# Kernel optimization log

Measured on AMD Instinct MI355X. Metric: run time of the kernel, lower is better.

Reference implementation:

```python
import jax, jax.numpy as jnp
import numpy as np

B, C, F_IN, F_OUT = 4096, 63, 250, 250
NEG_SLOPE = 0.2  # GATConv default negative_slope


def setup_inputs() -> dict:
    key = jax.random.key(0)
    ks = jax.random.split(key, 5)
    return {
        "x": jax.random.normal(ks[0], (B, 1, C, F_IN), dtype=jnp.float32),
        "W": jax.random.normal(ks[1], (F_IN, F_OUT), dtype=jnp.float32) / np.sqrt(F_IN),
        "att_src": jax.random.normal(ks[2], (F_OUT,), dtype=jnp.float32) / np.sqrt(F_OUT),
        "att_dst": jax.random.normal(ks[3], (F_OUT,), dtype=jnp.float32) / np.sqrt(F_OUT),
        "bias": jax.random.normal(ks[4], (F_OUT,), dtype=jnp.float32) * 0.01,
    }


def reference(x, W, att_src, att_dst, bias):
    # x: [B, 1, C, F_in] -> per-batch graph of C=63 nodes, fully connected
    # (all i!=j edges plus GATConv's default self-loops => dense C x C attention).
    h = jnp.einsum("bcf,fo->bco", x[:, 0], W)          # [B, C, F_out] node embeddings
    a_s = jnp.einsum("bco,o->bc", h, att_src)           # per-source score
    a_d = jnp.einsum("bco,o->bc", h, att_dst)           # per-destination score
    # e[b, dst, src] = leakyrelu(a_s[src] + a_d[dst]); softmax over sources per dst
    e = jax.nn.leaky_relu(a_s[:, None, :] + a_d[:, :, None], NEG_SLOPE)  # [B, C, C]
    alpha = jax.nn.softmax(e, axis=-1)
    out = jnp.einsum("bds,bso->bdo", alpha, h) + bias   # [B, C, F_out]
    return out[:, None]                                  # [B, 1, C, F_out]
```

## Files before the change

### kernel.cpp

```cpp
#include <hip/hip_runtime.h>
#include <hip/hip_bf16.h>

typedef __bf16 bf16;
typedef __attribute__((ext_vector_type(8))) __bf16 bf16x8;
typedef __attribute__((ext_vector_type(2))) __bf16 bf16x2;
typedef __attribute__((ext_vector_type(4))) float f32x4;
typedef __attribute__((ext_vector_type(4))) unsigned int uint4v;

#define C_NODES 63
#define F_DIM   250
#define NEG_SLOPE 0.2f
#define BS 8

#define ROWB      1040
#define SLAB      0
#define OFF_AS    65536
#define OFF_AD    65792
#define ALPHA_B   66048
#define LDS_BYTES 74240

__device__ __forceinline__ int swz(int a) { return a ^ ((a >> 3) & 0x70); }

typedef const __attribute__((address_space(1))) void* gas_t;
typedef __attribute__((address_space(3))) void* las_t;
__device__ __forceinline__ void dma16(const void* g, void* l) {
    __builtin_amdgcn_global_load_lds((gas_t)g, (las_t)l, 16, 0, 0);
}

__device__ __forceinline__ void bar_lgkm() {
    asm volatile("s_waitcnt lgkmcnt(0)" ::: "memory");
    __builtin_amdgcn_s_barrier();
    __builtin_amdgcn_sched_barrier(0);
}

extern "C" __global__ __launch_bounds__(256)
void gat_prep(const float* __restrict__ W, const float* __restrict__ att_src,
              const float* __restrict__ att_dst, bf16* __restrict__ Wp) {
    int i = blockIdx.x * 256 + threadIdx.x;
    int tile = i >> 9;
    int ln   = (i >> 3) & 63;
    int j    = i & 7;
    int kt = tile >> 4, nt = tile & 15;
    int k = kt * 32 + (ln >> 4) * 8 + j;
    int n = nt * 16 + (ln & 15);
    float v = 0.f;
    if (k < F_DIM) {
        if (n < F_DIM) {
            v = W[k * F_DIM + n];
        } else if (n == F_DIM || n == F_DIM + 1) {
            const float* att = (n == F_DIM) ? att_src : att_dst;
            float s = 0.f;
            for (int o = 0; o < F_DIM; ++o) s = fmaf(W[k * F_DIM + o], att[o], s);
            v = s;
        }
    }
    Wp[i] = (bf16)v;
}

extern "C" __global__ __launch_bounds__(512, 4)
void gat_main(const float* __restrict__ x, const bf16* __restrict__ Wp,
              const float* __restrict__ bias, float* __restrict__ out)
{
    __shared__ __align__(16) unsigned char smem[LDS_BYTES];
    const int tid  = threadIdx.x;
    const int lane = tid & 63;
    const int w    = tid >> 6;
    const int fl   = lane & 15;
    const int fh   = lane >> 4;
    const int b0   = blockIdx.x * BS;

    const bf16x8* wpv = (const bf16x8*)Wp;

    float bv0, bv1;
    { int f = w * 32 + fl;      bv0 = (f < F_DIM) ? bias[f] : 0.f;
      f += 16;                  bv1 = (f < F_DIM) ? bias[f] : 0.f; }

    if (tid < 63) {
        *(unsigned long long*)(smem + SLAB + tid * ROWB + 1000) = 0ull;
        *(f32x4*)(smem + SLAB + tid * ROWB + 1008) = (f32x4){0.f, 0.f, 0.f, 0.f};
    }

    {
        const float* xb = x + (size_t)b0 * (C_NODES * F_DIM);
        float2 tl = {0.f, 0.f};
        if (tid < 63) tl = *(const float2*)(xb + tid * F_DIM + 248);
#pragma unroll
        for (int rr = 0; rr < 8; ++rr) {
            int r = w * 8 + rr;
            if (r < 63 && lane < 62)
                dma16(xb + r * F_DIM + lane * 4, smem + SLAB + r * ROWB);
        }
        if (tid < 63) *(float2*)(smem + SLAB + tid * ROWB + 992) = tl;
    }
    asm volatile("s_waitcnt vmcnt(0)" ::: "memory");
    bar_lgkm();

#pragma unroll 1
    for (int i = 0; i < BS; ++i) {
        const int b = b0 + i;
        const float* xnext = x + (size_t)(b + 1) * (C_NODES * F_DIM);

        float2 tl = {0.f, 0.f};
        if (i + 1 < BS && tid < 63) tl = *(const float2*)(xnext + tid * F_DIM + 248);

        f32x4 acc[4][2];
#pragma unroll
        for (int mt = 0; mt < 4; ++mt) {
            acc[mt][0] = (f32x4){0.f, 0.f, 0.f, 0.f};
            acc[mt][1] = (f32x4){0.f, 0.f, 0.f, 0.f};
        }
#pragma unroll 1
        for (int kt = 0; kt < 8; ++kt) {
            bf16x8 bw0 = wpv[(kt * 16 + w * 2)     * 64 + lane];
            bf16x8 bw1 = wpv[(kt * 16 + w * 2 + 1) * 64 + lane];
#pragma unroll
            for (int mt = 0; mt < 4; ++mt) {
                int row = mt * 16 + fl;
                bf16x8 af;
                if (row < C_NODES) {
                    const f32x4* p = (const f32x4*)(smem + SLAB + row * ROWB + kt * 128 + fh * 32);
                    f32x4 lo = p[0], hi = p[1];
                    af = (bf16x8){ (bf16)lo.x, (bf16)lo.y, (bf16)lo.z, (bf16)lo.w,
                                   (bf16)hi.x, (bf16)hi.y, (bf16)hi.z, (bf16)hi.w };
                } else {
                    af = (bf16x8){(bf16)0.f,(bf16)0.f,(bf16)0.f,(bf16)0.f,
                                  (bf16)0.f,(bf16)0.f,(bf16)0.f,(bf16)0.f};
                }
                acc[mt][0] = __builtin_amdgcn_mfma_f32_16x16x32_bf16(af, bw0, acc[mt][0], 0, 0, 0);
                acc[mt][1] = __builtin_amdgcn_mfma_f32_16x16x32_bf16(af, bw1, acc[mt][1], 0, 0, 0);
            }
        }
        bar_lgkm();

        if (i + 1 < BS) {
#pragma unroll
            for (int rr = 0; rr < 8; ++rr) {
                int r = w * 8 + rr;
                if (r < 63 && lane < 62)
                    dma16(xnext + r * F_DIM + lane * 4, smem + SLAB + r * ROWB);
            }
        }
        if (w == 7 && (fl == 10 || fl == 11)) {
            float* dst = (float*)(smem + (fl == 10 ? OFF_AS : OFF_AD));
#pragma unroll
            for (int mt = 0; mt < 4; ++mt) {
                f32x4 v = acc[mt][1];
#pragma unroll
                for (int q = 0; q < 4; ++q) dst[mt * 16 + fh * 4 + q] = v[q];
            }
        }
        unsigned int pk[4][2][2];
#pragma unroll
        for (int mt = 0; mt < 4; ++mt)
#pragma unroll
            for (int nti = 0; nti < 2; ++nti) {
                f32x4 v = acc[mt][nti];
                bf16x2 p0 = { (bf16)v.x, (bf16)v.y };
                bf16x2 p1 = { (bf16)v.z, (bf16)v.w };
                pk[mt][nti][0] = __builtin_bit_cast(unsigned int, p0);
                pk[mt][nti][1] = __builtin_bit_cast(unsigned int, p1);
            }
        const int LA = ((fh & 1) << 5) + fl;
        const int LB = LA + 16;
        const bool fhHi = (fh & 2) != 0;
        uint4v hb[2][2];
#pragma unroll
        for (int nti = 0; nti < 2; ++nti)
#pragma unroll
            for (int kt2 = 0; kt2 < 2; ++kt2) {
                unsigned int u[4];
#pragma unroll
                for (int h = 0; h < 2; ++h) {
                    unsigned int a0 = __shfl(pk[kt2 * 2][nti][h],     LA);
                    unsigned int a1 = __shfl(pk[kt2 * 2 + 1][nti][h], LA);
                    u[h] = fhHi ? a1 : a0;
                    unsigned int c0 = __shfl(pk[kt2 * 2][nti][h],     LB);
                    unsigned int c1 = __shfl(pk[kt2 * 2 + 1][nti][h], LB);
                    u[2 + h] = fhHi ? c1 : c0;
                }
                hb[nti][kt2] = (uint4v){u[0], u[1], u[2], u[3]};
            }
        if (i + 1 < BS && tid < 63)
            *(float2*)(smem + SLAB + tid * ROWB + 992) = tl;
        bar_lgkm();

        {
            const float* AS  = (const float*)(smem + OFF_AS);
            const float* ADp = (const float*)(smem + OFF_AD);
            int d = tid >> 3;
            int c = tid & 7;
            float ad_v = ADp[d];
            f32x4 a0 = *(const f32x4*)(AS + c * 8);
            f32x4 a1 = *(const f32x4*)(AS + c * 8 + 4);
            float p[8];
#pragma unroll
            for (int k = 0; k < 4; ++k) {
                float e;
                e = a0[k] + ad_v; p[k]     = (e > 0.f) ? e : NEG_SLOPE * e;
                e = a1[k] + ad_v; p[4 + k] = (e > 0.f) ? e : NEG_SLOPE * e;
            }
            if (c == 7) p[7] = -3.0e38f;
            float md = p[0];
#pragma unroll
            for (int k = 1; k < 8; ++k) md = fmaxf(md, p[k]);
            md = fmaxf(md, __shfl_xor(md, 1));
            md = fmaxf(md, __shfl_xor(md, 2));
            md = fmaxf(md, __shfl_xor(md, 4));
            float sum = 0.f;
#pragma unroll
            for (int k = 0; k < 8; ++k) { p[k] = __expf(p[k] - md); sum += p[k]; }
            sum += __shfl_xor(sum, 1);
            sum += __shfl_xor(sum, 2);
            sum += __shfl_xor(sum, 4);
            float rz = 1.f / sum;
            bf16x8 pkv;
#pragma unroll
            for (int k = 0; k < 8; ++k) pkv[k] = (bf16)(p[k] * rz);
            *(bf16x8*)(smem + swz(ALPHA_B + d * 128 + c * 16)) = pkv;
        }
        bar_lgkm();

        f32x4 acc2[4][2];
#pragma unroll
        for (int mt = 0; mt < 4; ++mt) {
            acc2[mt][0] = (f32x4){0.f, 0.f, 0.f, 0.f};
            acc2[mt][1] = (f32x4){0.f, 0.f, 0.f, 0.f};
        }
#pragma unroll
        for (int ks = 0; ks < 2; ++ks) {
            int kk = ks * 32 + fh * 8;
            bf16x8 h0 = __builtin_bit_cast(bf16x8, hb[0][ks]);
            bf16x8 h1 = __builtin_bit_cast(bf16x8, hb[1][ks]);
#pragma unroll
            for (int mt = 0; mt < 4; ++mt) {
                bf16x8 aal = *(const bf16x8*)(smem + swz(ALPHA_B + (mt * 16 + fl) * 128 + kk * 2));
                acc2[mt][0] = __builtin_amdgcn_mfma_f32_16x16x32_bf16(aal, h0, acc2[mt][0], 0, 0, 0);
                acc2[mt][1] = __builtin_amdgcn_mfma_f32_16x16x32_bf16(aal, h1, acc2[mt][1], 0, 0, 0);
            }
        }
        float* ob = out + (size_t)b * (C_NODES * F_DIM);
#pragma unroll
        for (int mt = 0; mt < 4; ++mt) {
#pragma unroll
            for (int q = 0; q < 4; ++q) {
                int r = mt * 16 + fh * 4 + q;
                if (r < C_NODES) {
                    int f = w * 32 + fl;
                    ob[r * F_DIM + f] = acc2[mt][0][q] + bv0;
                    f += 16;
                    if (f < F_DIM) ob[r * F_DIM + f] = acc2[mt][1][q] + bv1;
                }
            }
        }
        if (i + 1 < BS) {
            asm volatile("s_waitcnt vmcnt(32)" ::: "memory");
            bar_lgkm();
        }
    }
}

extern "C" void kernel_launch(void* const* d_in, const int* in_sizes, int n_in,
                              void* d_out, int out_size, void* d_ws, size_t ws_size,
                              hipStream_t stream) {
    const float* x       = (const float*)d_in[0];
    const float* W       = (const float*)d_in[1];
    const float* att_src = (const float*)d_in[2];
    const float* att_dst = (const float*)d_in[3];
    const float* bias    = (const float*)d_in[4];
    float* out = (float*)d_out;
    bf16* Wp = (bf16*)d_ws;

    gat_prep<<<256, 256, 0, stream>>>(W, att_src, att_dst, Wp);
    gat_main<<<512, 512, 0, stream>>>(x, Wp, bias, out);
}
```

Before: 137.9 us.

## Drop a per-batch barrier, reuse accumulators, and unroll the projection k-loop by two

Moves the attention-score LDS writes ahead of the first barrier and defers the x-tail store to just before the softmax barrier. This removes one workgroup barrier per batch element. The second GEMM now reuses the first GEMM's accumulator registers to lower register pressure, and the K loop of the projection GEMM is unrolled by two. The x-tail store now overlaps the in-flight async DMA into the same slab rows, which makes correctness depend on the rows not colliding.

```diff
diff --git a/kernel.cpp b/kernel.cpp
--- a/kernel.cpp
+++ b/kernel.cpp
@@ -82,15 +82,15 @@
 
     {
         const float* xb = x + (size_t)b0 * (C_NODES * F_DIM);
-        float2 tl = {0.f, 0.f};
-        if (tid < 63) tl = *(const float2*)(xb + tid * F_DIM + 248);
+        float2 tl0 = {0.f, 0.f};
+        if (tid < 63) tl0 = *(const float2*)(xb + tid * F_DIM + 248);
 #pragma unroll
         for (int rr = 0; rr < 8; ++rr) {
             int r = w * 8 + rr;
             if (r < 63 && lane < 62)
                 dma16(xb + r * F_DIM + lane * 4, smem + SLAB + r * ROWB);
         }
-        if (tid < 63) *(float2*)(smem + SLAB + tid * ROWB + 992) = tl;
+        if (tid < 63) *(float2*)(smem + SLAB + tid * ROWB + 992) = tl0;
     }
     asm volatile("s_waitcnt vmcnt(0)" ::: "memory");
     bar_lgkm();
@@ -103,13 +103,13 @@
         float2 tl = {0.f, 0.f};
         if (i + 1 < BS && tid < 63) tl = *(const float2*)(xnext + tid * F_DIM + 248);
 
-        f32x4 acc[4][2];
+        f32x4 gacc[4][2];
 #pragma unroll
         for (int mt = 0; mt < 4; ++mt) {
-            acc[mt][0] = (f32x4){0.f, 0.f, 0.f, 0.f};
-            acc[mt][1] = (f32x4){0.f, 0.f, 0.f, 0.f};
-        }
-#pragma unroll 1
+            gacc[mt][0] = (f32x4){0.f, 0.f, 0.f, 0.f};
+            gacc[mt][1] = (f32x4){0.f, 0.f, 0.f, 0.f};
+        }
+#pragma unroll 2
         for (int kt = 0; kt < 8; ++kt) {
             bf16x8 bw0 = wpv[(kt * 16 + w * 2)     * 64 + lane];
             bf16x8 bw1 = wpv[(kt * 16 + w * 2 + 1) * 64 + lane];
@@ -126,8 +126,17 @@
                     af = (bf16x8){(bf16)0.f,(bf16)0.f,(bf16)0.f,(bf16)0.f,
                                   (bf16)0.f,(bf16)0.f,(bf16)0.f,(bf16)0.f};
                 }
-                acc[mt][0] = __builtin_amdgcn_mfma_f32_16x16x32_bf16(af, bw0, acc[mt][0], 0, 0, 0);
-                acc[mt][1] = __builtin_amdgcn_mfma_f32_16x16x32_bf16(af, bw1, acc[mt][1], 0, 0, 0);
+                gacc[mt][0] = __builtin_amdgcn_mfma_f32_16x16x32_bf16(af, bw0, gacc[mt][0], 0, 0, 0);
+                gacc[mt][1] = __builtin_amdgcn_mfma_f32_16x16x32_bf16(af, bw1, gacc[mt][1], 0, 0, 0);
+            }
+        }
+        if (w == 7 && (fl == 10 || fl == 11)) {
+            float* dst = (float*)(smem + (fl == 10 ? OFF_AS : OFF_AD));
+#pragma unroll
+            for (int mt = 0; mt < 4; ++mt) {
+                f32x4 v = gacc[mt][1];
+#pragma unroll
+                for (int q = 0; q < 4; ++q) dst[mt * 16 + fh * 4 + q] = v[q];
             }
         }
         bar_lgkm();
@@ -140,21 +149,12 @@
                     dma16(xnext + r * F_DIM + lane * 4, smem + SLAB + r * ROWB);
             }
         }
-        if (w == 7 && (fl == 10 || fl == 11)) {
-            float* dst = (float*)(smem + (fl == 10 ? OFF_AS : OFF_AD));
-#pragma unroll
-            for (int mt = 0; mt < 4; ++mt) {
-                f32x4 v = acc[mt][1];
-#pragma unroll
-                for (int q = 0; q < 4; ++q) dst[mt * 16 + fh * 4 + q] = v[q];
-            }
-        }
         unsigned int pk[4][2][2];
 #pragma unroll
         for (int mt = 0; mt < 4; ++mt)
 #pragma unroll
             for (int nti = 0; nti < 2; ++nti) {
-                f32x4 v = acc[mt][nti];
+                f32x4 v = gacc[mt][nti];
                 bf16x2 p0 = { (bf16)v.x, (bf16)v.y };
                 bf16x2 p1 = { (bf16)v.z, (bf16)v.w };
                 pk[mt][nti][0] = __builtin_bit_cast(unsigned int, p0);
@@ -180,10 +180,6 @@
                 }
                 hb[nti][kt2] = (uint4v){u[0], u[1], u[2], u[3]};
             }
-        if (i + 1 < BS && tid < 63)
-            *(float2*)(smem + SLAB + tid * ROWB + 992) = tl;
-        bar_lgkm();
-
         {
             const float* AS  = (const float*)(smem + OFF_AS);
             const float* ADp = (const float*)(smem + OFF_AD);
@@ -218,13 +214,14 @@
             for (int k = 0; k < 8; ++k) pkv[k] = (bf16)(p[k] * rz);
             *(bf16x8*)(smem + swz(ALPHA_B + d * 128 + c * 16)) = pkv;
         }
+        if (i + 1 < BS && tid < 63)
+            *(float2*)(smem + SLAB + tid * ROWB + 992) = tl;
         bar_lgkm();
 
-        f32x4 acc2[4][2];
 #pragma unroll
         for (int mt = 0; mt < 4; ++mt) {
-            acc2[mt][0] = (f32x4){0.f, 0.f, 0.f, 0.f};
-            acc2[mt][1] = (f32x4){0.f, 0.f, 0.f, 0.f};
+            gacc[mt][0] = (f32x4){0.f, 0.f, 0.f, 0.f};
+            gacc[mt][1] = (f32x4){0.f, 0.f, 0.f, 0.f};
         }
 #pragma unroll
         for (int ks = 0; ks < 2; ++ks) {
@@ -234,8 +231,8 @@
 #pragma unroll
             for (int mt = 0; mt < 4; ++mt) {
                 bf16x8 aal = *(const bf16x8*)(smem + swz(ALPHA_B + (mt * 16 + fl) * 128 + kk * 2));
-                acc2[mt][0] = __builtin_amdgcn_mfma_f32_16x16x32_bf16(aal, h0, acc2[mt][0], 0, 0, 0);
-                acc2[mt][1] = __builtin_amdgcn_mfma_f32_16x16x32_bf16(aal, h1, acc2[mt][1], 0, 0, 0);
+                gacc[mt][0] = __builtin_amdgcn_mfma_f32_16x16x32_bf16(aal, h0, gacc[mt][0], 0, 0, 0);
+                gacc[mt][1] = __builtin_amdgcn_mfma_f32_16x16x32_bf16(aal, h1, gacc[mt][1], 0, 0, 0);
             }
         }
         float* ob = out + (size_t)b * (C_NODES * F_DIM);
@@ -246,9 +243,9 @@
                 int r = mt * 16 + fh * 4 + q;
                 if (r < C_NODES) {
                     int f = w * 32 + fl;
-                    ob[r * F_DIM + f] = acc2[mt][0][q] + bv0;
+                    ob[r * F_DIM + f] = gacc[mt][0][q] + bv0;
                     f += 16;
-                    if (f < F_DIM) ob[r * F_DIM + f] = acc2[mt][1][q] + bv1;
+                    if (f < F_DIM) ob[r * F_DIM + f] = gacc[mt][1][q] + bv1;
                 }
             }
         }
```

Result: no change. 139.6 us (+1.2%).
